# Kernel tuning notes

Measured on AMD Instinct MI355X. Metric: run time of the kernel, lower is better.

The kernel has to match this reference:

```python
import jax, jax.numpy as jnp
import numpy as np

L1, L2, N, C = 4096, 4096, 8, 3


def setup_inputs() -> dict:
    key = jax.random.key(0)
    k1, k2 = jax.random.split(key)
    coords1 = jax.random.uniform(k1, (L1, N, C), dtype=jnp.float32)
    coords2 = jax.random.uniform(k2, (L2, N, C), dtype=jnp.float32)
    return {"coords1": coords1, "coords2": coords2}


def reference(coords1, coords2):
    # coords1: [L1, N, C], coords2: [L2, N, C]
    l1, n, c = coords1.shape
    l2 = coords2.shape[0]
    # Batch-first layout, matching flatten_batch semantics (per-batch NN only)
    q = jnp.swapaxes(coords2, 0, 1)  # [N, L2, C] query points
    r = jnp.swapaxes(coords1, 0, 1)  # [N, L1, C] reference points
    # Squared euclidean distances per batch: [N, L2, L1]
    d2 = (
        jnp.sum(q * q, axis=-1)[:, :, None]
        + jnp.sum(r * r, axis=-1)[:, None, :]
        - 2.0 * jnp.einsum("nlc,nmc->nlm", q, r)
    )
    # tc.nearest returns global flat index; original does fmod(L1) to get the
    # per-batch index — argmin within each batch gives that directly.
    nearest = jnp.argmin(d2, axis=-1)  # [N, L2]
    clusters = nearest.T  # [L2, N]
    # torch.meshgrid(arange(L2), arange(N)) with 'ij' indexing; indices[-1] is
    # the batch index broadcast to [L2, N].
    batch_idx = jnp.broadcast_to(jnp.arange(n, dtype=jnp.int64 if False else jnp.int32), (l2, n))
    return (clusters.reshape(-1), batch_idx.reshape(-1))
```

## Files before the change

kernel.cpp:

```cpp
#include <hip/hip_runtime.h>
#include <float.h>


constexpr int kL1 = 4096, kL2 = 4096, kN = 8;
constexpr int kCS = 520;
constexpr size_t kOffPts = 8ull * kCS * 4;
constexpr size_t kOffIdx = kOffPts + 8ull * kL1 * 16;
constexpr size_t kWsBytes = kOffIdx + 8ull * kL1 * 4;

__device__ __forceinline__ float rr_exact(float x, float y, float z) {
  return __fadd_rn(__fadd_rn(__fmul_rn(x, x), __fmul_rn(y, y)), __fmul_rn(z, z));
}

__global__ __launch_bounds__(1024)
void bin_kernel(const float* __restrict__ c1, int* __restrict__ cellStart,
                float4* __restrict__ pts, int* __restrict__ pidx) {
#pragma clang fp contract(off)
  __shared__ int cnt[512];
  const int tid = threadIdx.x;
  const int n = blockIdx.x;
  if (tid < 512) cnt[tid] = 0;
  __syncthreads();

  float xs[4], ys[4], zs[4];
  int cl[4];
#pragma unroll
  for (int k = 0; k < 4; ++k) {
    const int j = k * 1024 + tid;
    const float* p = c1 + (j * kN + n) * 3;
    const float x = p[0], y = p[1], z = p[2];
    xs[k] = x; ys[k] = y; zs[k] = z;
    const int cx = min(7, max(0, (int)(x * 8.0f)));
    const int cy = min(7, max(0, (int)(y * 8.0f)));
    const int cz = min(7, max(0, (int)(z * 8.0f)));
    cl[k] = (cz * 8 + cy) * 8 + cx;
    atomicAdd(&cnt[cl[k]], 1);
  }
  __syncthreads();

  if (tid < 64) {
    int loc[8], part = 0;
#pragma unroll
    for (int i = 0; i < 8; ++i) { loc[i] = cnt[tid * 8 + i]; part += loc[i]; }
    int inc = part;
#pragma unroll
    for (int off = 1; off < 64; off <<= 1) {
      const int v = __shfl_up(inc, off);
      if (tid >= off) inc += v;
    }
    int base = inc - part;
#pragma unroll
    for (int i = 0; i < 8; ++i) {
      const int c = tid * 8 + i;
      cellStart[n * kCS + c] = base;
      cnt[c] = base;
      base += loc[i];
    }
    if (tid == 0) cellStart[n * kCS + 512] = kL1;
  }
  __syncthreads();

#pragma unroll
  for (int k = 0; k < 4; ++k) {
    const int j = k * 1024 + tid;
    const int pos = atomicAdd(&cnt[cl[k]], 1);
    pts[n * kL1 + pos] = make_float4(xs[k], ys[k], zs[k], rr_exact(xs[k], ys[k], zs[k]));
    pidx[n * kL1 + pos] = j;
  }
}

__global__ __launch_bounds__(256, 8)
void grid_nn_kernel(const int* __restrict__ cellStart, const float4* __restrict__ pts,
                    const int* __restrict__ pidx, const float* __restrict__ c2,
                    int* __restrict__ out) {
#pragma clang fp contract(off)
  const int gid = blockIdx.x * 256 + threadIdx.x;
  const int query = gid >> 3;
  const int sub = gid & 7;
  const int qj = query >> 3;
  const int n = query & 7;

  const float* p = c2 + (qj * kN + n) * 3;
  const float qx = p[0], qy = p[1], qz = p[2];
  const float qq = rr_exact(qx, qy, qz);
  const int cx = min(7, max(0, (int)(qx * 8.0f)));
  const int cy = min(7, max(0, (int)(qy * 8.0f)));
  const int cz = min(7, max(0, (int)(qz * 8.0f)));

  const int* __restrict__ cs = cellStart + n * kCS;
  const float4* __restrict__ P = pts + n * kL1;
  const int* __restrict__ I = pidx + n * kL1;

  float bd = FLT_MAX;
  int bi = 0x7FFFFFFF;

  for (int r = 0; r < 8; ++r) {
    if (r > 0) {
      const float t = (r - 1) * 0.125f;
      if (t * t > __fadd_rn(bd, 4e-6f)) break;
    }
    for (int dz = -r; dz <= r; ++dz) {
      const int z = cz + dz;
      if (z < 0 || z > 7) continue;
      const bool zf = (dz == r || dz == -r);
      for (int dy = -r; dy <= r; ++dy) {
        const int y = cy + dy;
        if (y < 0 || y > 7) continue;
        const bool zyf = zf || dy == r || dy == -r;
        for (int dx = -r; dx <= r; ++dx) {
          if (!zyf && dx != r && dx != -r) continue;
          const int x = cx + dx;
          if (x < 0 || x > 7) continue;
          const int c = (z * 8 + y) * 8 + x;
          const int s = cs[c], e = cs[c + 1];
          for (int pp = s + sub; pp < e; pp += 8) {
            const float4 rp = P[pp];
            const int id = I[pp];
            const float dot = __fadd_rn(
                __fadd_rn(__fmul_rn(qx, rp.x), __fmul_rn(qy, rp.y)),
                __fmul_rn(qz, rp.z));
            const float d2 = __fmaf_rn(-2.0f, dot, __fadd_rn(qq, rp.w));
            if (d2 < bd || (d2 == bd && id < bi)) { bd = d2; bi = id; }
          }
        }
      }
    }
#pragma unroll
    for (int m = 1; m <= 4; m <<= 1) {
      const float od = __shfl_xor(bd, m);
      const int oi = __shfl_xor(bi, m);
      if (od < bd || (od == bd && oi < bi)) { bd = od; bi = oi; }
    }
  }

  if (sub == 0) {
    out[qj * kN + n] = bi;
    out[kL2 * kN + qj * kN + n] = n;
  }
}

constexpr int kQPerBlock = 16;
constexpr int kQ = 4;
constexpr int kChunk = 1024;

__global__ __launch_bounds__(256, 4)
void nearest_kernel_lds(const float* __restrict__ c1, const float* __restrict__ c2,
                        int* __restrict__ out) {
#pragma clang fp contract(off)
  __shared__ float sRx[kChunk], sRy[kChunk], sRz[kChunk], sRr[kChunk];
  const int tid = threadIdx.x;
  const int n = blockIdx.y;
  const int wave = tid >> 6;
  const int lane = tid & 63;
  const int q0 = blockIdx.x * kQPerBlock + wave * kQ;

  float qxs[kQ], qys[kQ], qzs[kQ], qqs[kQ];
#pragma unroll
  for (int i = 0; i < kQ; ++i) {
    const float* p = c2 + ((q0 + i) * kN + n) * 3;
    qxs[i] = p[0]; qys[i] = p[1]; qzs[i] = p[2];
    qqs[i] = rr_exact(qxs[i], qys[i], qzs[i]);
  }
  float bd[kQ]; int bt[kQ];
#pragma unroll
  for (int i = 0; i < kQ; ++i) { bd[i] = FLT_MAX; bt[i] = 0; }

  for (int chunk = 0; chunk < kL1 / kChunk; ++chunk) {
    __syncthreads();
    {
      const int jb = chunk * kChunk + tid * 4;
      float x[4], y[4], z[4], w4[4];
#pragma unroll
      for (int k = 0; k < 4; ++k) {
        const float* p = c1 + ((jb + k) * kN + n) * 3;
        x[k] = p[0]; y[k] = p[1]; z[k] = p[2];
        w4[k] = rr_exact(x[k], y[k], z[k]);
      }
      *reinterpret_cast<float4*>(&sRx[tid * 4]) = make_float4(x[0], x[1], x[2], x[3]);
      *reinterpret_cast<float4*>(&sRy[tid * 4]) = make_float4(y[0], y[1], y[2], y[3]);
      *reinterpret_cast<float4*>(&sRz[tid * 4]) = make_float4(z[0], z[1], z[2], z[3]);
      *reinterpret_cast<float4*>(&sRr[tid * 4]) = make_float4(w4[0], w4[1], w4[2], w4[3]);
    }
    __syncthreads();
#pragma unroll
    for (int t = 0; t < kChunk / 256; ++t) {
      const int tg = chunk * (kChunk / 256) + t;
      const int base = t * 256 + lane * 4;
      const float4 x4 = *reinterpret_cast<const float4*>(&sRx[base]);
      const float4 y4 = *reinterpret_cast<const float4*>(&sRy[base]);
      const float4 z4 = *reinterpret_cast<const float4*>(&sRz[base]);
      const float4 r4 = *reinterpret_cast<const float4*>(&sRr[base]);
      const float xs[4] = {x4.x, x4.y, x4.z, x4.w};
      const float ys[4] = {y4.x, y4.y, y4.z, y4.w};
      const float zs[4] = {z4.x, z4.y, z4.z, z4.w};
      const float rs[4] = {r4.x, r4.y, r4.z, r4.w};
#pragma unroll
      for (int i = 0; i < kQ; ++i) {
        float d[4];
#pragma unroll
        for (int k = 0; k < 4; ++k) {
          const float dot = __fadd_rn(
              __fadd_rn(__fmul_rn(qxs[i], xs[k]), __fmul_rn(qys[i], ys[k])),
              __fmul_rn(qzs[i], zs[k]));
          d[k] = __fmaf_rn(-2.0f, dot, __fadd_rn(qqs[i], rs[k]));
        }
        const float old = bd[i];
        float m = fminf(fminf(d[0], d[1]), old);
        m = fminf(fminf(d[2], d[3]), m);
        bd[i] = m;
        if (m < old) bt[i] = tg;
      }
    }
  }
  int sel[kQ];
#pragma unroll
  for (int i = 0; i < kQ; ++i) sel[i] = bt[i] * 64 + lane;
#pragma unroll
  for (int m = 1; m <= 32; m <<= 1) {
#pragma unroll
    for (int i = 0; i < kQ; ++i) {
      const float od = __shfl_xor(bd[i], m);
      const int os = __shfl_xor(sel[i], m);
      if (od < bd[i] || (od == bd[i] && os < sel[i])) { bd[i] = od; sel[i] = os; }
    }
  }
#pragma unroll
  for (int i = 0; i < kQ; ++i) {
    if (lane == i) {
      const int j0 = sel[i] * 4;
      float best = FLT_MAX; int kk = 0;
#pragma unroll
      for (int k = 0; k < 4; ++k) {
        const float* p = c1 + ((j0 + k) * kN + n) * 3;
        const float r0 = p[0], r1 = p[1], r2 = p[2];
        const float rr = rr_exact(r0, r1, r2);
        const float dot = __fadd_rn(
            __fadd_rn(__fmul_rn(qxs[i], r0), __fmul_rn(qys[i], r1)),
            __fmul_rn(qzs[i], r2));
        const float dc = __fmaf_rn(-2.0f, dot, __fadd_rn(qqs[i], rr));
        if (dc < best) { best = dc; kk = k; }
      }
      out[(q0 + i) * kN + n] = j0 + kk;
      out[kL2 * kN + (q0 + i) * kN + n] = n;
    }
  }
}

extern "C" void kernel_launch(void* const* d_in, const int* in_sizes, int n_in,
                              void* d_out, int out_size, void* d_ws, size_t ws_size,
                              hipStream_t stream) {
  const float* c1 = (const float*)d_in[0];
  const float* c2 = (const float*)d_in[1];
  int* out = (int*)d_out;
  if (d_ws != nullptr && ws_size >= kWsBytes) {
    int* cellStart = (int*)d_ws;
    float4* pts = (float4*)((char*)d_ws + kOffPts);
    int* pidx = (int*)((char*)d_ws + kOffIdx);
    bin_kernel<<<dim3(kN), dim3(1024), 0, stream>>>(c1, cellStart, pts, pidx);
    grid_nn_kernel<<<dim3(kL2 * kN * 8 / 256), dim3(256), 0, stream>>>(
        cellStart, pts, pidx, c2, out);
  } else {
    dim3 grid(kL2 / kQPerBlock, kN);
    nearest_kernel_lds<<<grid, dim3(256), 0, stream>>>(c1, c2, out);
  }
}
```

Measured before the change: 85.88 us.

## Search 3x3x3 neighborhood with full wave per query, fall back to brute force

Replaces the expanding-shell grid search (8 lanes per query) with a fixed 3x3x3 cell neighborhood scanned by a full 64-lane wave per query, using contiguous x-runs per row. If the best distance cannot be proven within the neighborhood, the wave falls back to a full scan of all reference points in the batch. The point index is packed into the float4 w component and |r|^2 is recomputed on the fly, which removes the separate index array and its load. This trades fewer loop branches and loads for more lanes per query and a costly brute-force fallback when neighbors are far.

```diff
diff --git a/kernel.cpp b/kernel.cpp
--- a/kernel.cpp
+++ b/kernel.cpp
@@ -5,8 +5,7 @@
 constexpr int kL1 = 4096, kL2 = 4096, kN = 8;
 constexpr int kCS = 520;
 constexpr size_t kOffPts = 8ull * kCS * 4;
-constexpr size_t kOffIdx = kOffPts + 8ull * kL1 * 16;
-constexpr size_t kWsBytes = kOffIdx + 8ull * kL1 * 4;
+constexpr size_t kWsBytes = kOffPts + 8ull * kL1 * 16;
 
 __device__ __forceinline__ float rr_exact(float x, float y, float z) {
   return __fadd_rn(__fadd_rn(__fmul_rn(x, x), __fmul_rn(y, y)), __fmul_rn(z, z));
@@ -14,7 +13,7 @@
 
 __global__ __launch_bounds__(1024)
 void bin_kernel(const float* __restrict__ c1, int* __restrict__ cellStart,
-                float4* __restrict__ pts, int* __restrict__ pidx) {
+                float4* __restrict__ pts) {
 #pragma clang fp contract(off)
   __shared__ int cnt[512];
   const int tid = threadIdx.x;
@@ -64,21 +63,19 @@
   for (int k = 0; k < 4; ++k) {
     const int j = k * 1024 + tid;
     const int pos = atomicAdd(&cnt[cl[k]], 1);
-    pts[n * kL1 + pos] = make_float4(xs[k], ys[k], zs[k], rr_exact(xs[k], ys[k], zs[k]));
-    pidx[n * kL1 + pos] = j;
+    pts[n * kL1 + pos] =
+        make_float4(xs[k], ys[k], zs[k], __int_as_float(j));
   }
 }
 
 __global__ __launch_bounds__(256, 8)
 void grid_nn_kernel(const int* __restrict__ cellStart, const float4* __restrict__ pts,
-                    const int* __restrict__ pidx, const float* __restrict__ c2,
-                    int* __restrict__ out) {
+                    const float* __restrict__ c2, int* __restrict__ out) {
 #pragma clang fp contract(off)
-  const int gid = blockIdx.x * 256 + threadIdx.x;
-  const int query = gid >> 3;
-  const int sub = gid & 7;
-  const int qj = query >> 3;
-  const int n = query & 7;
+  const int n = blockIdx.y;
+  const int wave = threadIdx.x >> 6;
+  const int lane = threadIdx.x & 63;
+  const int qj = blockIdx.x * 4 + wave;
 
   const float* p = c2 + (qj * kN + n) * 3;
   const float qx = p[0], qy = p[1], qz = p[2];
@@ -86,54 +83,63 @@
   const int cx = min(7, max(0, (int)(qx * 8.0f)));
   const int cy = min(7, max(0, (int)(qy * 8.0f)));
   const int cz = min(7, max(0, (int)(qz * 8.0f)));
+  const int xlo = max(0, cx - 1), xhi = min(7, cx + 1);
 
   const int* __restrict__ cs = cellStart + n * kCS;
   const float4* __restrict__ P = pts + n * kL1;
-  const int* __restrict__ I = pidx + n * kL1;
 
   float bd = FLT_MAX;
   int bi = 0x7FFFFFFF;
 
-  for (int r = 0; r < 8; ++r) {
-    if (r > 0) {
-      const float t = (r - 1) * 0.125f;
-      if (t * t > __fadd_rn(bd, 4e-6f)) break;
-    }
-    for (int dz = -r; dz <= r; ++dz) {
-      const int z = cz + dz;
-      if (z < 0 || z > 7) continue;
-      const bool zf = (dz == r || dz == -r);
-      for (int dy = -r; dy <= r; ++dy) {
-        const int y = cy + dy;
-        if (y < 0 || y > 7) continue;
-        const bool zyf = zf || dy == r || dy == -r;
-        for (int dx = -r; dx <= r; ++dx) {
-          if (!zyf && dx != r && dx != -r) continue;
-          const int x = cx + dx;
-          if (x < 0 || x > 7) continue;
-          const int c = (z * 8 + y) * 8 + x;
-          const int s = cs[c], e = cs[c + 1];
-          for (int pp = s + sub; pp < e; pp += 8) {
-            const float4 rp = P[pp];
-            const int id = I[pp];
-            const float dot = __fadd_rn(
-                __fadd_rn(__fmul_rn(qx, rp.x), __fmul_rn(qy, rp.y)),
-                __fmul_rn(qz, rp.z));
-            const float d2 = __fmaf_rn(-2.0f, dot, __fadd_rn(qq, rp.w));
-            if (d2 < bd || (d2 == bd && id < bi)) { bd = d2; bi = id; }
-          }
-        }
-      }
-    }
-#pragma unroll
-    for (int m = 1; m <= 4; m <<= 1) {
+#pragma unroll
+  for (int dz = -1; dz <= 1; ++dz) {
+#pragma unroll
+    for (int dy = -1; dy <= 1; ++dy) {
+      const int z = cz + dz, y = cy + dy;
+      if (z < 0 || z > 7 || y < 0 || y > 7) continue;
+      const int row = (z * 8 + y) * 8;
+      const int s = cs[row + xlo];
+      const int e = cs[row + xhi + 1];
+      for (int pp = s + lane; pp < e; pp += 64) {
+        const float4 rp = P[pp];
+        const int id = __float_as_int(rp.w);
+        const float rr = rr_exact(rp.x, rp.y, rp.z);
+        const float dot = __fadd_rn(
+            __fadd_rn(__fmul_rn(qx, rp.x), __fmul_rn(qy, rp.y)),
+            __fmul_rn(qz, rp.z));
+        const float d2 = __fmaf_rn(-2.0f, dot, __fadd_rn(qq, rr));
+        if (d2 < bd || (d2 == bd && id < bi)) { bd = d2; bi = id; }
+      }
+    }
+  }
+
+#pragma unroll
+  for (int m = 1; m <= 32; m <<= 1) {
+    const float od = __shfl_xor(bd, m);
+    const int oi = __shfl_xor(bi, m);
+    if (od < bd || (od == bd && oi < bi)) { bd = od; bi = oi; }
+  }
+
+  if (!(0.015625f > __fadd_rn(bd, 4e-6f))) {
+    for (int pp = lane; pp < kL1; pp += 64) {
+      const float4 rp = P[pp];
+      const int id = __float_as_int(rp.w);
+      const float rr = rr_exact(rp.x, rp.y, rp.z);
+      const float dot = __fadd_rn(
+          __fadd_rn(__fmul_rn(qx, rp.x), __fmul_rn(qy, rp.y)),
+          __fmul_rn(qz, rp.z));
+      const float d2 = __fmaf_rn(-2.0f, dot, __fadd_rn(qq, rr));
+      if (d2 < bd || (d2 == bd && id < bi)) { bd = d2; bi = id; }
+    }
+#pragma unroll
+    for (int m = 1; m <= 32; m <<= 1) {
       const float od = __shfl_xor(bd, m);
       const int oi = __shfl_xor(bi, m);
       if (od < bd || (od == bd && oi < bi)) { bd = od; bi = oi; }
     }
   }
 
-  if (sub == 0) {
+  if (lane == 0) {
     out[qj * kN + n] = bi;
     out[kL2 * kN + qj * kN + n] = n;
   }
@@ -255,10 +261,9 @@
   if (d_ws != nullptr && ws_size >= kWsBytes) {
     int* cellStart = (int*)d_ws;
     float4* pts = (float4*)((char*)d_ws + kOffPts);
-    int* pidx = (int*)((char*)d_ws + kOffIdx);
-    bin_kernel<<<dim3(kN), dim3(1024), 0, stream>>>(c1, cellStart, pts, pidx);
-    grid_nn_kernel<<<dim3(kL2 * kN * 8 / 256), dim3(256), 0, stream>>>(
-        cellStart, pts, pidx, c2, out);
+    bin_kernel<<<dim3(kN), dim3(1024), 0, stream>>>(c1, cellStart, pts);
+    grid_nn_kernel<<<dim3(kL2 / 4, kN), dim3(256), 0, stream>>>(
+        cellStart, pts, c2, out);
   } else {
     dim3 grid(kL2 / kQPerBlock, kN);
     nearest_kernel_lds<<<grid, dim3(256), 0, stream>>>(c1, c2, out);
```

Result: slower. 88.02 us (+2.5%).
